# Optimization experiments

Hardware: AMD Instinct MI355X
Metric: run time of the kernel (lower is better)

## Reference

```python
import jax, jax.numpy as jnp
import numpy as np

NUM_IT = 5            # init_kwargs num_it
N_NODES = 200_000
N_EDGES = 6_400_000   # avg degree 32
N_INIT_COLORS = 16

# odd 32-bit mixing constants (Knuth / xxhash primes); uint32 mults wrap mod 2^32
M1 = np.uint32(2654435761)
M2 = np.uint32(2246822519)
M3 = np.uint32(3266489917)
M4 = np.uint32(668265263)


def setup_inputs() -> dict:
    key = jax.random.key(0)
    k1, k2 = jax.random.split(key)
    x = jax.random.randint(k1, (N_NODES,), 0, N_INIT_COLORS, dtype=jnp.int32)
    edge_index = jax.random.randint(k2, (2, N_EDGES), 0, N_NODES, dtype=jnp.int32)
    return {"x": x, "edge_index": edge_index}


def _wl_iteration(colors, row, col, num_nodes):
    """One WLConv step: new color = id of (own color, sorted multiset of neighbor colors).

    The torch WLConv sorts each node's neighbor colors, hashes the tuple, and
    assigns compact ids via a dict. Here we do the same math vectorized:
    lexsort edges by (row, neighbor color), compute a position-weighted 2x32-bit
    hash of the sorted per-node sequence via segment_sum, mix in the node's own
    color, then relabel distinct keys to compact ids 0..k-1 with jnp.unique.
    """
    E = row.shape[0]
    c = colors[col]                                   # neighbor colors per edge [E]
    order = jnp.lexsort((c, row))                     # sort by node, then by color
    r_s = row[order]                                  # [E] sorted rows
    c_s = c[order].astype(jnp.uint32)                 # [E] sorted neighbor colors

    ones = jnp.ones((E,), dtype=jnp.int32)
    deg = jax.ops.segment_sum(ones, row, num_segments=num_nodes)      # [N]
    start = jnp.cumsum(deg) - deg                                     # segment offsets [N]
    pos = (jnp.arange(E, dtype=jnp.int32) - start[r_s]).astype(jnp.uint32)  # rank within node

    # two independent position-weighted hash lanes over each sorted neighbor list
    lane1 = jax.ops.segment_sum((c_s + 1) * (pos * M1 + M2), r_s, num_segments=num_nodes)
    lane2 = jax.ops.segment_sum((c_s + 1) * (pos * M3 + M4), r_s, num_segments=num_nodes)

    own = colors.astype(jnp.uint32) + 1
    key2 = jnp.stack([lane1 * M2 + own * M1, lane2 * M4 + own * M3], axis=1)  # [N,2]

    # dict-style relabeling: distinct keys -> compact ids (at most N distinct)
    _, inv = jnp.unique(key2, axis=0, size=num_nodes, return_inverse=True,
                        fill_value=jnp.uint32(0))
    return inv.reshape(-1).astype(colors.dtype)


def reference(x, edge_index):
    row, col = edge_index[0], edge_index[1]
    colors = x.astype(jnp.int32)
    for _ in range(NUM_IT):  # fixed small layer loop, not a data-dim loop
        colors = _wl_iteration(colors, row, col, N_NODES)
    return colors
```

## Files before the change

kernel.cpp:

```cpp
#include <hip/hip_runtime.h>
#include <stdint.h>

typedef unsigned int u32;
typedef unsigned long long u64;

#define M1 2654435761u
#define M2 2246822519u
#define M3 3266489917u
#define M4 668265263u
#define NUM_IT 5
#define PCHUNK 16384
#define HCH 65536
#define TILE 4096
#define PBCH 4096
#define CCAP 16384
#define SB 64
#define CHB 33
#define NKB 2048
#define KSH 53
#define SLOT 256


__global__ void k_init(const int* __restrict__ x, int* __restrict__ colors,
                       u32* __restrict__ cnt5, u32* __restrict__ bhist,
                       u32* __restrict__ cnt3, int n, int nbuck) {
    int i = blockIdx.x * blockDim.x + threadIdx.x;
    if (i < n) colors[i] = x[i];
    if (i < NUM_IT * NKB * 16) cnt5[i] = 0u;
    if (i >= 165888 && i < 165888 + nbuck) bhist[i - 165888] = 0u;
    if (i >= 168960 && i < 168960 + 48) cnt3[i - 168960] = 0u;
}

__global__ void k_chist(const int* __restrict__ row, u32* __restrict__ bhist,
                        u32* __restrict__ thist, int e, int nbuck) {
    __shared__ u32 fineh[1024];
    __shared__ u32 shist[16 * SB];
    int t = threadIdx.x;
    fineh[t] = 0u;
    shist[t] = 0u;
    __syncthreads();
    int c0 = blockIdx.x * HCH;
    int ce = c0 + HCH; if (ce > e) ce = e;
    int k = 0;
    for (int i = c0 + t; i < ce; i += 1024, ++k) {
        u32 r = (u32)row[i];
        atomicAdd(&fineh[r >> 8], 1u);
        atomicAdd(&shist[((k >> 2) << 6) | (r >> 12)], 1u);
    }
    __syncthreads();
    if (t < nbuck) {
        u32 v = fineh[t];
        if (v) atomicAdd(&bhist[t], v);
    }
    {
        int m = t >> 6;
        if (c0 + m * TILE < e)
            thist[(size_t)(blockIdx.x * 16 + m) * SB + (t & 63)] = shist[t];
    }
}

__global__ void k_cscan(const u32* __restrict__ bhist, u32* __restrict__ boffE,
                        u32* __restrict__ bcur, u32* __restrict__ boffS,
                        int nbuck, int nbS) {
    __shared__ u32 sh[256];
    u32 run = 0u;
    for (int base = 0; base < nbuck; base += 256) {
        int id = base + threadIdx.x;
        u32 x = (id < nbuck) ? bhist[id] : 0u;
        sh[threadIdx.x] = x;
        __syncthreads();
        for (int o = 1; o < 256; o <<= 1) {
            u32 t = (threadIdx.x >= (u32)o) ? sh[threadIdx.x - o] : 0u;
            __syncthreads();
            sh[threadIdx.x] += t;
            __syncthreads();
        }
        if (id < nbuck) {
            u32 excl = sh[threadIdx.x] - x + run;
            boffE[id] = excl;
            bcur[id] = excl;
            if ((id & 15) == 0) boffS[id >> 4] = excl;
        }
        u32 tot = sh[255];
        __syncthreads();
        run += tot;
    }
    if (threadIdx.x == 0) { boffE[nbuck] = run; boffS[nbS] = run; }
}

__global__ void k_tscan(const u32* __restrict__ thist, const u32* __restrict__ boffS,
                        u32* __restrict__ tbase, int ntiles) {
    __shared__ u32 sh[256];
    int b = blockIdx.x;
    int t = threadIdx.x;
    u32 run = boffS[b];
    for (int base = 0; base < ntiles; base += 256) {
        int tile = base + t;
        u32 x = (tile < ntiles) ? thist[(size_t)tile * SB + b] : 0u;
        sh[t] = x;
        __syncthreads();
        for (int o = 1; o < 256; o <<= 1) {
            u32 y = (t >= o) ? sh[t - o] : 0u;
            __syncthreads();
            sh[t] += y;
            __syncthreads();
        }
        if (tile < ntiles) tbase[(size_t)tile * SB + b] = run + sh[t] - x;
        u32 tot = sh[255];
        __syncthreads();
        run += tot;
    }
}

__global__ void k_partA(const int* __restrict__ row, const int* __restrict__ col,
                        const u32* __restrict__ thist, const u32* __restrict__ tbase,
                        u32* __restrict__ adjt, int e) {
    __shared__ u32 vals[TILE];
    __shared__ unsigned char bkt[TILE];
    __shared__ u32 lbase[SB + 1], gbase[SB], cur[SB];
    int t = threadIdx.x;
    int c0 = blockIdx.x * TILE;
    int ce = c0 + TILE; if (ce > e) ce = e;
    if (t < SB) {
        gbase[t] = tbase[(size_t)blockIdx.x * SB + t];
        cur[t] = 0u;
        lbase[t] = thist[(size_t)blockIdx.x * SB + t];
    }
    __syncthreads();
    if (t == 0) {
        u32 run = 0u;
        for (int b = 0; b < SB; ++b) { u32 h = lbase[b]; lbase[b] = run; run += h; }
        lbase[SB] = run;
    }
    __syncthreads();
    for (int i = c0 + t; i < ce; i += 256) {
        u32 r = (u32)row[i];
        u32 s = r >> 12;
        u32 p = lbase[s] + atomicAdd(&cur[s], 1u);
        vals[p] = ((r & 4095u) << 18) | (u32)col[i];
        bkt[p] = (unsigned char)s;
    }
    __syncthreads();
    int cnt = ce - c0;
    for (int i = t; i < cnt; i += 256) {
        u32 b = (u32)bkt[i];
        adjt[gbase[b] + ((u32)i - lbase[b])] = vals[i];
    }
}

__global__ void k_partB(const u32* __restrict__ adjt, const u32* __restrict__ boffS,
                        u32* __restrict__ ecur, u32* __restrict__ adj) {
    __shared__ u32 vals[PBCH];
    __shared__ u32 hist[16], lbase[17], gbase[16], cur[16];
    int s = blockIdx.x / CHB, c = blockIdx.x % CHB;
    u32 lo = boffS[s] + (u32)c * PBCH;
    u32 hi = boffS[s + 1];
    if (lo >= hi) return;
    if (hi > lo + PBCH) hi = lo + PBCH;
    int t = threadIdx.x;
    if (t < 16) hist[t] = 0u;
    __syncthreads();
    for (u32 i = lo + t; i < hi; i += 256)
        atomicAdd(&hist[(adjt[i] >> 26) & 15u], 1u);
    __syncthreads();
    if (t == 0) {
        u32 run = 0u;
        for (int b = 0; b < 16; ++b) { lbase[b] = run; run += hist[b]; }
        lbase[16] = run;
    }
    __syncthreads();
    if (t < 16) {
        u32 h = hist[t];
        gbase[t] = h ? atomicAdd(&ecur[s * 16 + t], h) : 0u;
        cur[t] = 0u;
    }
    __syncthreads();
    for (u32 i = lo + t; i < hi; i += 256) {
        u32 v = adjt[i];
        u32 b = (v >> 26) & 15u;
        vals[lbase[b] + atomicAdd(&cur[b], 1u)] = v;
    }
    __syncthreads();
    u32 cnt = hi - lo;
    for (u32 i = t; i < cnt; i += 256) {
        u32 v = vals[i];
        u32 b = (v >> 26) & 15u;
        adj[gbase[b] + (i - lbase[b])] = v & 0x03FFFFFFu;
    }
}

__global__ void k_part(const int* __restrict__ row, const int* __restrict__ col,
                       u32* __restrict__ bcur, u32* __restrict__ adjp, int e, int nbuck) {
    __shared__ u32 hist[1024], base[1024], cur[1024];
    int c0 = blockIdx.x * PCHUNK;
    int cend = c0 + PCHUNK; if (cend > e) cend = e;
    for (int t = threadIdx.x; t < nbuck; t += 256) hist[t] = 0u;
    __syncthreads();
    for (int i = c0 + threadIdx.x; i < cend; i += 256)
        atomicAdd(&hist[((u32)row[i]) >> 8], 1u);
    __syncthreads();
    for (int t = threadIdx.x; t < nbuck; t += 256) {
        u32 h = hist[t];
        base[t] = h ? atomicAdd(&bcur[t], h) : 0u;
        cur[t] = 0u;
    }
    __syncthreads();
    for (int i = c0 + threadIdx.x; i < cend; i += 256) {
        u32 r = (u32)row[i];
        u32 b = r >> 8;
        u32 local = atomicAdd(&cur[b], 1u);
        adjp[base[b] + local] = ((r & 255u) << 18) | (u32)col[i];
    }
}

__global__ void k_csr(u32* __restrict__ adj, const u32* __restrict__ boffE,
                      u32* __restrict__ deg, u32* __restrict__ start,
                      u64* __restrict__ lists, u32* __restrict__ cnt3, int n) {
    __shared__ u32 buf[CCAP];
    __shared__ u32 cnt[256], cur[256];
    __shared__ u32 wsum[4];
    __shared__ u32 ch[3], cbase[3];
    int b = blockIdx.x;
    int v0 = b << 8;
    u32 bs = boffE[b], be = boffE[b + 1];
    int c = (int)(be - bs);
    if (c > CCAP) c = CCAP;
    int t = threadIdx.x;
    int lane = t & 63, w = t >> 6;
    if (t < 256) cnt[t] = 0u;
    if (t < 3) ch[t] = 0u;
    for (int i = t; i < c; i += 1024) buf[i] = adj[bs + i];
    __syncthreads();
    for (int i = t; i < c; i += 1024)
        atomicAdd(&cnt[buf[i] >> 18], 1u);
    __syncthreads();
    u32 myc = 0u, ps = 0u;
    if (t < 256) {
        myc = cnt[t];
        ps = myc;
#pragma unroll
        for (int o = 1; o < 64; o <<= 1) {
            u32 y = (u32)__shfl_up((int)ps, o, 64);
            if (lane >= o) ps += y;
        }
        if (lane == 63) wsum[w] = ps;
    }
    __syncthreads();
    u32 cls = 0u, crk = 0u, myStart = 0u;
    int v = v0 + t;
    if (t < 256) {
        u32 wb = 0u;
        for (int j = 0; j < w; ++j) wb += wsum[j];
        u32 excl = wb + ps - myc;
        myStart = bs + excl;
        if (v < n) {
            deg[v] = myc;
            start[v] = myStart;
            cls = (myc <= 32u) ? 0u : ((myc <= 64u) ? 1u : 2u);
            crk = atomicAdd(&ch[cls], 1u);
        }
        cur[t] = myStart;
    }
    __syncthreads();
    if (t < 3) cbase[t] = ch[t] ? atomicAdd(&cnt3[t * 16], ch[t]) : 0u;
    __syncthreads();
    if (t < 256 && v < n) {
        u32 dcl = myc > 0x3FFFu ? 0x3FFFu : myc;
        lists[cls * (size_t)n + cbase[cls] + crk] =
            ((u64)((dcl << 18) | (u32)v) << 32) | (u64)myStart;
    }
    for (int i = t; i < c; i += 1024) {
        u32 p = buf[i];
        u32 q = atomicAdd(&cur[p >> 18], 1u);
        adj[q] = p & 0x3FFFFu;
    }
}


__device__ __forceinline__ void ce_reg(u32& a, u32& b, bool up) {
    u32 mn = a < b ? a : b, mx = a < b ? b : a;
    a = up ? mn : mx; b = up ? mx : mn;
}
__device__ __forceinline__ void ce_shf(u32& a, int o, bool tm) {
    u32 ot = (u32)__shfl_xor((int)a, o, 64);
    u32 mn = a < ot ? a : ot, mx = a < ot ? ot : a;
    a = tm ? mn : mx;
}
#define CE_SH4(o, tm) { ce_shf(c0, o, tm); ce_shf(c1, o, tm); ce_shf(c2, o, tm); ce_shf(c3, o, tm); }
#define CE_RG4(up)    { ce_reg(c0, c2, up); ce_reg(c1, c3, up); ce_reg(c0, c1, up); ce_reg(c2, c3, up); }

__global__ void k_hash(const int* __restrict__ colors, const u32* __restrict__ deg,
                       const u32* __restrict__ adj,
                       const u64* __restrict__ lists, const u32* __restrict__ cnt3,
                       u64* __restrict__ keys, int n) {
    int lane = threadIdx.x & 63;
    int wid = (int)((blockIdx.x * 256u + threadIdx.x) >> 6);
    u32 nA = cnt3[0], nBc = cnt3[16], nCc = cnt3[32];
    int octA = (int)((nA + 7u) >> 3);
    int quadB = (int)((nBc + 3u) >> 2);
    if (wid < octA) {
        int s = lane & 7;
        int li = 8 * wid + (lane >> 3);
        int node = -1;
        u32 c0 = 0xFFFFFFFFu, c1 = 0xFFFFFFFFu, c2 = 0xFFFFFFFFu, c3 = 0xFFFFFFFFu;
        u32 e0 = 4u * (u32)s;
        if (li < (int)nA) {
            u64 pk = lists[li];
            u32 st = (u32)pk;
            u32 hi = (u32)(pk >> 32);
            u32 d = hi >> 18;
            node = (int)(hi & 0x3FFFFu);
            if (e0 + 0u < d) c0 = (u32)colors[adj[st + e0 + 0u]];
            if (e0 + 1u < d) c1 = (u32)colors[adj[st + e0 + 1u]];
            if (e0 + 2u < d) c2 = (u32)colors[adj[st + e0 + 2u]];
            if (e0 + 3u < d) c3 = (u32)colors[adj[st + e0 + 3u]];
        }
        bool s1 = (s & 1) == 0, s2 = (s & 2) == 0, s4 = (s & 4) == 0;
        ce_reg(c0, c1, true); ce_reg(c2, c3, false);
        CE_RG4(s1)
        CE_SH4(1, s1 == s2)
        CE_RG4(s2)
        CE_SH4(2, s2 == s4)
        CE_SH4(1, s1 == s4)
        CE_RG4(s4)
        CE_SH4(4, s4)
        CE_SH4(2, s2)
        CE_SH4(1, s1)
        CE_RG4(true)
        u32 a1 = e0 * M1, a3 = e0 * M3;
        u32 v = (c0 + 1u) * (a1 + M2)           + (c1 + 1u) * (a1 + 1u * M1 + M2)
              + (c2 + 1u) * (a1 + 2u * M1 + M2) + (c3 + 1u) * (a1 + 3u * M1 + M2);
        u32 w = (c0 + 1u) * (a3 + M4)           + (c1 + 1u) * (a3 + 1u * M3 + M4)
              + (c2 + 1u) * (a3 + 2u * M3 + M4) + (c3 + 1u) * (a3 + 3u * M3 + M4);
#pragma unroll
        for (int o = 1; o < 8; o <<= 1) {
            v += (u32)__shfl_xor((int)v, o, 64);
            w += (u32)__shfl_xor((int)w, o, 64);
        }
        if (s == 0 && node >= 0) {
            u32 own = (u32)colors[node] + 1u;
            keys[node] = ((u64)(v * M2 + own * M1) << 32) | (u64)(w * M4 + own * M3);
        }
    } else if (wid < octA + quadB) {
        int s = lane & 15;
        int li = 4 * (wid - octA) + (lane >> 4);
        int node = -1;
        u32 c0 = 0xFFFFFFFFu, c1 = 0xFFFFFFFFu, c2 = 0xFFFFFFFFu, c3 = 0xFFFFFFFFu;
        u32 e0 = 4u * (u32)s;
        if (li < (int)nBc) {
            u64 pk = lists[(size_t)n + (u32)li];
            u32 st = (u32)pk;
            u32 hi = (u32)(pk >> 32);
            u32 d = hi >> 18;
            node = (int)(hi & 0x3FFFFu);
            if (e0 + 0u < d) c0 = (u32)colors[adj[st + e0 + 0u]];
            if (e0 + 1u < d) c1 = (u32)colors[adj[st + e0 + 1u]];
            if (e0 + 2u < d) c2 = (u32)colors[adj[st + e0 + 2u]];
            if (e0 + 3u < d) c3 = (u32)colors[adj[st + e0 + 3u]];
        }
        bool s1 = (s & 1) == 0, s2 = (s & 2) == 0, s4 = (s & 4) == 0, s8 = (s & 8) == 0;
        ce_reg(c0, c1, true); ce_reg(c2, c3, false);
        CE_RG4(s1)
        CE_SH4(1, s1 == s2)
        CE_RG4(s2)
        CE_SH4(2, s2 == s4)
        CE_SH4(1, s1 == s4)
        CE_RG4(s4)
        CE_SH4(4, s4 == s8)
        CE_SH4(2, s2 == s8)
        CE_SH4(1, s1 == s8)
        CE_RG4(s8)
        CE_SH4(8, s8)
        CE_SH4(4, s4)
        CE_SH4(2, s2)
        CE_SH4(1, s1)
        CE_RG4(true)
        u32 a1 = e0 * M1, a3 = e0 * M3;
        u32 v = (c0 + 1u) * (a1 + M2)           + (c1 + 1u) * (a1 + 1u * M1 + M2)
              + (c2 + 1u) * (a1 + 2u * M1 + M2) + (c3 + 1u) * (a1 + 3u * M1 + M2);
        u32 w = (c0 + 1u) * (a3 + M4)           + (c1 + 1u) * (a3 + 1u * M3 + M4)
              + (c2 + 1u) * (a3 + 2u * M3 + M4) + (c3 + 1u) * (a3 + 3u * M3 + M4);
#pragma unroll
        for (int o = 1; o < 16; o <<= 1) {
            v += (u32)__shfl_xor((int)v, o, 64);
            w += (u32)__shfl_xor((int)w, o, 64);
        }
        if (s == 0 && node >= 0) {
            u32 own = (u32)colors[node] + 1u;
            keys[node] = ((u64)(v * M2 + own * M1) << 32) | (u64)(w * M4 + own * M3);
        }
    } else if (wid < octA + quadB + (int)nCc) {
        u64 pk = lists[2u * (size_t)n + (u32)(wid - octA - quadB)];
        int node = (int)((u32)(pk >> 32) & 0x3FFFFu);
        u32 st = (u32)pk;
        u32 d = deg[node];
        u32 v = 0u, w = 0u;
        for (u32 i = (u32)lane; i < d; i += 64u) {
            u32 ci = (u32)colors[adj[st + i]];
            u32 pos = 0u;
            for (u32 j = 0; j < d; ++j) {
                u32 cj = (u32)colors[adj[st + j]];
                pos += (cj < ci) || (cj == ci && j < i);
            }
            v += (ci + 1u) * (pos * M1 + M2);
            w += (ci + 1u) * (pos * M3 + M4);
        }
        for (int o = 32; o > 0; o >>= 1) {
            v += (u32)__shfl_xor((int)v, o, 64);
            w += (u32)__shfl_xor((int)w, o, 64);
        }
        if (lane == 0) {
            u32 own = (u32)colors[node] + 1u;
            keys[node] = ((u64)(v * M2 + own * M1) << 32) | (u64)(w * M4 + own * M3);
        }
    }
}


__global__ void k_scatter(const u64* __restrict__ keys, u64* __restrict__ out,
                          u32* __restrict__ nout, u32* __restrict__ cnt, int n) {
    int i = blockIdx.x * 256 + threadIdx.x;
    if (i >= n) return;
    u64 k = keys[i];
    u32 b = (u32)(k >> KSH);
    u32 r = atomicAdd(&cnt[b * 16], 1u);
    if (r < (u32)SLOT) {
        u32 p = (b << 8) + r;
        out[p] = k;
        nout[p] = (u32)i;
    }
}

__global__ void k_bsort(u64* __restrict__ data, u32* __restrict__ nidx,
                        const u32* __restrict__ cnt,
                        u32* __restrict__ comb, u32* __restrict__ dcount) {
    __shared__ u64 sh[256];
    __shared__ u32 pid[256];
    __shared__ u32 ts[256];
    int b = blockIdx.x;
    u32 lo = (u32)b << 8;
    int c = (int)cnt[b * 16];
    if (c > SLOT) c = SLOT;
    int m = (c <= 128) ? 128 : 256;
    int t = threadIdx.x;
    for (int i = t; i < m; i += 256) {
        sh[i] = (i < c) ? data[lo + i] : ~0ULL;
        pid[i] = (i < c) ? nidx[lo + i] : 0u;
    }
    __syncthreads();
    for (int k = 2; k <= m; k <<= 1) {
        for (int j = k >> 1; j > 0; j >>= 1) {
            for (int e = t; e < m; e += 256) {
                int p = e ^ j;
                if (p > e) {
                    u64 a = sh[e], cc = sh[p];
                    bool up = ((e & k) == 0);
                    if (up ? (a > cc) : (a < cc)) {
                        sh[e] = cc; sh[p] = a;
                        u32 tp = pid[e]; pid[e] = pid[p]; pid[p] = tp;
                    }
                }
            }
            __syncthreads();
        }
    }
    int i0 = 2 * t, i1 = 2 * t + 1;
    u32 f0 = (i0 < c) ? ((i0 == 0) ? 1u : (sh[i0] != sh[i0 - 1] ? 1u : 0u)) : 0u;
    u32 f1 = (i1 < c) ? (sh[i1] != sh[i1 - 1] ? 1u : 0u) : 0u;
    u32 s2 = f0 + f1;
    ts[t] = s2;
    __syncthreads();
    for (int o = 1; o < 256; o <<= 1) {
        u32 x = (t >= o) ? ts[t - o] : 0u;
        __syncthreads();
        ts[t] += x;
        __syncthreads();
    }
    u32 excl = ts[t] - s2;
    if (i0 < c) { nidx[lo + i0] = pid[i0]; comb[lo + i0] = excl + f0; }
    if (i1 < c) { nidx[lo + i1] = pid[i1]; comb[lo + i1] = excl + f0 + f1; }
    if (t == 255) dcount[b] = ts[255];
}

__global__ void k_relabel(const u32* __restrict__ comb, const u32* __restrict__ nidx,
                          const u32* __restrict__ dcount, const u32* __restrict__ cnt,
                          int* __restrict__ colors) {
    __shared__ u32 red[256];
    int b = blockIdx.x;
    int t = threadIdx.x;
    u32 partial = 0u;
    for (int j = t; j < b; j += 256) partial += dcount[j];
    red[t] = partial;
    __syncthreads();
    for (int o = 128; o > 0; o >>= 1) {
        if (t < o) red[t] += red[t + o];
        __syncthreads();
    }
    u32 dbase = red[0];
    u32 c = cnt[b * 16];
    if (c > (u32)SLOT) c = (u32)SLOT;
    u32 lo = (u32)b << 8;
    for (u32 i = (u32)t; i < c; i += 256u)
        colors[nidx[lo + i]] = (int)(dbase + comb[lo + i] - 1u);
}


extern "C" void kernel_launch(void* const* d_in, const int* in_sizes, int n_in,
                              void* d_out, int out_size, void* d_ws, size_t ws_size,
                              hipStream_t stream) {
    const int* x = (const int*)d_in[0];
    const int* ei = (const int*)d_in[1];
    const int N = in_sizes[0];
    const int E = in_sizes[1] / 2;
    const int* row = ei;
    const int* col = ei + E;
    int* colors = (int*)d_out;

    const int ntiles = (E + TILE - 1) / TILE;

    char* ws = (char*)d_ws;
    size_t off = 0;
#define WS_ALLOC(T, name, bytes) T name = (T)(ws + off); off += (((size_t)(bytes)) + 255) & ~(size_t)255;
    WS_ALLOC(u32*, deg, (size_t)N * 4)
    WS_ALLOC(u32*, start, (size_t)N * 4)
    WS_ALLOC(u32*, adj, (size_t)E * 4)
    WS_ALLOC(u64*, keys, (size_t)N * 8)
    WS_ALLOC(u64*, sorted, (size_t)NKB * SLOT * 8)
    WS_ALLOC(u32*, nidx, (size_t)NKB * SLOT * 4)
    WS_ALLOC(u32*, comb, (size_t)NKB * SLOT * 4)
    WS_ALLOC(u64*, lists, (size_t)3 * N * 8)
    WS_ALLOC(u32*, cnt5, (size_t)NUM_IT * NKB * 16 * 4)
    WS_ALLOC(u32*, dcount, NKB * 4)
    WS_ALLOC(u32*, bhist, 1024 * 4)
    WS_ALLOC(u32*, boffE, 1025 * 4)
    WS_ALLOC(u32*, bcur, 1024 * 4)
    WS_ALLOC(u32*, boffS, (SB + 1) * 4)
    WS_ALLOC(u32*, cnt3, 48 * 4)
    WS_ALLOC(u32*, thist, (size_t)ntiles * SB * 4)
    WS_ALLOC(u32*, tbase, (size_t)ntiles * SB * 4)
    u32* adjt = (u32*)(ws + off);
    const bool two_level = (off + (size_t)E * 4 <= ws_size);
#undef WS_ALLOC

    const int nB = (N + 255) / 256;
    const int nbuck = (N + 255) >> 8;
    const int nbS = (nbuck + 15) >> 4;

    k_init<<<nB, 256, 0, stream>>>(x, colors, cnt5, bhist, cnt3, N, nbuck);
    k_chist<<<(E + HCH - 1) / HCH, 1024, 0, stream>>>(row, bhist, thist, E, nbuck);
    k_cscan<<<1, 256, 0, stream>>>(bhist, boffE, bcur, boffS, nbuck, nbS);
    if (two_level) {
        k_tscan<<<nbS, 256, 0, stream>>>(thist, boffS, tbase, ntiles);
        k_partA<<<ntiles, 256, 0, stream>>>(row, col, thist, tbase, adjt, E);
        k_partB<<<nbS * CHB, 256, 0, stream>>>(adjt, boffS, bcur, adj);
    } else {
        k_part<<<(E + PCHUNK - 1) / PCHUNK, 256, 0, stream>>>(row, col, bcur, adj, E, nbuck);
    }
    k_csr<<<nbuck, 1024, 0, stream>>>(adj, boffE, deg, start, lists, cnt3, N);

    for (int it = 0; it < NUM_IT; ++it) {
        u32* cnt_it = cnt5 + (size_t)it * NKB * 16;
        k_hash<<<(N + 3) / 4, 256, 0, stream>>>(colors, deg, adj, lists, cnt3, keys, N);
        k_scatter<<<nB, 256, 0, stream>>>(keys, sorted, nidx, cnt_it, N);
        k_bsort<<<NKB, 256, 0, stream>>>(sorted, nidx, cnt_it, comb, dcount);
        k_relabel<<<NKB, 256, 0, stream>>>(comb, nidx, dcount, cnt_it, colors);
    }
}
```

Before: 594.6 us.

## Replace node-index permutation with per-node binary search into sorted key buckets

The bucket sort no longer carries a node-index payload. Sorted keys are written back, and relabeling becomes a per-node gather: each node binary-searches its key inside its bucket to find its compact id. Each relabel block also recomputes the bucket base offsets with a wavefront prefix scan over 2048 counts, replacing the per-bucket serial partial sums. This removes the nidx traffic and the scattered color writes, in exchange for extra binary-search reads (about 8 steps) and a redundant scan in every block.

```diff
diff --git a/kernel.cpp b/kernel.cpp
--- a/kernel.cpp
+++ b/kernel.cpp
@@ -418,24 +418,18 @@
 
 
 __global__ void k_scatter(const u64* __restrict__ keys, u64* __restrict__ out,
-                          u32* __restrict__ nout, u32* __restrict__ cnt, int n) {
+                          u32* __restrict__ cnt, int n) {
     int i = blockIdx.x * 256 + threadIdx.x;
     if (i >= n) return;
     u64 k = keys[i];
     u32 b = (u32)(k >> KSH);
     u32 r = atomicAdd(&cnt[b * 16], 1u);
-    if (r < (u32)SLOT) {
-        u32 p = (b << 8) + r;
-        out[p] = k;
-        nout[p] = (u32)i;
-    }
-}
-
-__global__ void k_bsort(u64* __restrict__ data, u32* __restrict__ nidx,
-                        const u32* __restrict__ cnt,
+    if (r < (u32)SLOT) out[(b << 8) + r] = k;
+}
+
+__global__ void k_bsort(u64* __restrict__ data, const u32* __restrict__ cnt,
                         u32* __restrict__ comb, u32* __restrict__ dcount) {
     __shared__ u64 sh[256];
-    __shared__ u32 pid[256];
     __shared__ u32 ts[256];
     int b = blockIdx.x;
     u32 lo = (u32)b << 8;
@@ -443,10 +437,8 @@
     if (c > SLOT) c = SLOT;
     int m = (c <= 128) ? 128 : 256;
     int t = threadIdx.x;
-    for (int i = t; i < m; i += 256) {
+    for (int i = t; i < m; i += 256)
         sh[i] = (i < c) ? data[lo + i] : ~0ULL;
-        pid[i] = (i < c) ? nidx[lo + i] : 0u;
-    }
     __syncthreads();
     for (int k = 2; k <= m; k <<= 1) {
         for (int j = k >> 1; j > 0; j >>= 1) {
@@ -455,10 +447,7 @@
                 if (p > e) {
                     u64 a = sh[e], cc = sh[p];
                     bool up = ((e & k) == 0);
-                    if (up ? (a > cc) : (a < cc)) {
-                        sh[e] = cc; sh[p] = a;
-                        u32 tp = pid[e]; pid[e] = pid[p]; pid[p] = tp;
-                    }
+                    if (up ? (a > cc) : (a < cc)) { sh[e] = cc; sh[p] = a; }
                 }
             }
             __syncthreads();
@@ -477,31 +466,44 @@
         __syncthreads();
     }
     u32 excl = ts[t] - s2;
-    if (i0 < c) { nidx[lo + i0] = pid[i0]; comb[lo + i0] = excl + f0; }
-    if (i1 < c) { nidx[lo + i1] = pid[i1]; comb[lo + i1] = excl + f0 + f1; }
+    if (i0 < c) { data[lo + i0] = sh[i0]; comb[lo + i0] = excl + f0; }
+    if (i1 < c) { data[lo + i1] = sh[i1]; comb[lo + i1] = excl + f0 + f1; }
     if (t == 255) dcount[b] = ts[255];
 }
 
-__global__ void k_relabel(const u32* __restrict__ comb, const u32* __restrict__ nidx,
-                          const u32* __restrict__ dcount, const u32* __restrict__ cnt,
-                          int* __restrict__ colors) {
-    __shared__ u32 red[256];
-    int b = blockIdx.x;
-    int t = threadIdx.x;
-    u32 partial = 0u;
-    for (int j = t; j < b; j += 256) partial += dcount[j];
-    red[t] = partial;
-    __syncthreads();
-    for (int o = 128; o > 0; o >>= 1) {
-        if (t < o) red[t] += red[t + o];
-        __syncthreads();
-    }
-    u32 dbase = red[0];
+__global__ void k_relabel(const u64* __restrict__ keys, const u64* __restrict__ data,
+                          const u32* __restrict__ comb, const u32* __restrict__ dcount,
+                          const u32* __restrict__ cnt, int* __restrict__ colors, int n) {
+    __shared__ u32 dbaseL[NKB];
+    int t = threadIdx.x;
+    if (t < 64) {
+        u32 v[32]; u32 s = 0u;
+#pragma unroll
+        for (int i = 0; i < 32; ++i) { v[i] = dcount[t * 32 + i]; s += v[i]; }
+        u32 ps = s;
+#pragma unroll
+        for (int o = 1; o < 64; o <<= 1) {
+            u32 y = (u32)__shfl_up((int)ps, o, 64);
+            if (t >= o) ps += y;
+        }
+        u32 run = ps - s;
+#pragma unroll
+        for (int i = 0; i < 32; ++i) { dbaseL[t * 32 + i] = run; run += v[i]; }
+    }
+    __syncthreads();
+    int i = blockIdx.x * 256 + t;
+    if (i >= n) return;
+    u64 k = keys[i];
+    u32 b = (u32)(k >> KSH);
+    u32 lo = (u32)b << 8;
     u32 c = cnt[b * 16];
     if (c > (u32)SLOT) c = (u32)SLOT;
-    u32 lo = (u32)b << 8;
-    for (u32 i = (u32)t; i < c; i += 256u)
-        colors[nidx[lo + i]] = (int)(dbase + comb[lo + i] - 1u);
+    u32 lb = 0u, ub = c;
+    while (lb < ub) {
+        u32 mid = (lb + ub) >> 1;
+        if (data[lo + mid] < k) lb = mid + 1; else ub = mid;
+    }
+    colors[i] = (int)(dbaseL[b] + comb[lo + lb] - 1u);
 }
 
 
@@ -526,7 +528,6 @@
     WS_ALLOC(u32*, adj, (size_t)E * 4)
     WS_ALLOC(u64*, keys, (size_t)N * 8)
     WS_ALLOC(u64*, sorted, (size_t)NKB * SLOT * 8)
-    WS_ALLOC(u32*, nidx, (size_t)NKB * SLOT * 4)
     WS_ALLOC(u32*, comb, (size_t)NKB * SLOT * 4)
     WS_ALLOC(u64*, lists, (size_t)3 * N * 8)
     WS_ALLOC(u32*, cnt5, (size_t)NUM_IT * NKB * 16 * 4)
@@ -561,8 +562,8 @@
     for (int it = 0; it < NUM_IT; ++it) {
         u32* cnt_it = cnt5 + (size_t)it * NKB * 16;
         k_hash<<<(N + 3) / 4, 256, 0, stream>>>(colors, deg, adj, lists, cnt3, keys, N);
-        k_scatter<<<nB, 256, 0, stream>>>(keys, sorted, nidx, cnt_it, N);
-        k_bsort<<<NKB, 256, 0, stream>>>(sorted, nidx, cnt_it, comb, dcount);
-        k_relabel<<<NKB, 256, 0, stream>>>(comb, nidx, dcount, cnt_it, colors);
-    }
-}
+        k_scatter<<<nB, 256, 0, stream>>>(keys, sorted, cnt_it, N);
+        k_bsort<<<NKB, 256, 0, stream>>>(sorted, cnt_it, comb, dcount);
+        k_relabel<<<nB, 256, 0, stream>>>(keys, sorted, comb, dcount, cnt_it, colors, N);
+    }
+}
```

Result: slower. 606.9 us (+2.1%).
